# Performance work log

Measured on AMD Instinct MI355X. Metric: run time of the kernel, lower is better.

Reference implementation:

```python
import jax, jax.numpy as jnp
import numpy as np

TEMPERATURE = 0.07
EPS = 1e-12  # F.normalize eps


def _l2norm(x):
    n = jnp.linalg.norm(x, axis=-1, keepdims=True)
    return x / jnp.maximum(n, EPS)


def setup_inputs() -> dict:
    key = jax.random.key(0)
    k1, k2 = jax.random.split(key)
    B, T, H = 16, 512, 1024
    h_source = jax.random.normal(k1, (B, T, H), dtype=jnp.float32)
    h_target = jax.random.normal(k2, (B, T, H), dtype=jnp.float32)
    src_mask = jnp.ones((B, T), dtype=bool)
    tgt_mask = jnp.ones((B, T), dtype=bool)
    return {"h_source": h_source, "h_target": h_target,
            "src_mask": src_mask, "tgt_mask": tgt_mask}


def reference(h_source, h_target, src_mask, tgt_mask):
    # Masks are all-True and B*T == max_samples, so boolean selection == reshape
    # and the random subsampling branch is never taken (deterministic path).
    H = h_source.shape[-1]
    h_s = h_source.reshape(-1, H).astype(jnp.float32)          # (N, H)
    h_t = jax.lax.stop_gradient(h_target.reshape(-1, H)).astype(jnp.float32)  # detached

    h_s_norm = _l2norm(h_s)                                     # (N, H)
    h_t_norm = _l2norm(h_t)                                     # (M, H)
    sim = h_s_norm @ h_t_norm.T                                 # (N, M) cosine sim

    pos_idx = jnp.argmax(sim, axis=1)                           # == topk_idx[:, 0]
    logits = sim / TEMPERATURE
    # cross-entropy with pos_idx labels (stable log-softmax)
    logp = jax.nn.log_softmax(logits, axis=1)
    l_contrastive = -jnp.mean(jnp.take_along_axis(logp, pos_idx[:, None], axis=1)[:, 0])

    # contextual consistency: adjacent source tokens' NN embeddings should align
    nn_embeds = h_t_norm[pos_idx]                               # (N, H)
    nn_sim = jnp.sum(nn_embeds[:-1] * nn_embeds[1:], axis=-1)   # (N-1,)
    l_contextual = 1.0 - jnp.mean(nn_sim)

    return (l_contrastive, l_contextual)
```

## Files before the change

### kernel.cpp

```cpp
#include <hip/hip_runtime.h>
#include <hip/hip_bf16.h>
#include <stdint.h>


#define HDIM 1024
#define NROW 8192
#define TEMP_INV (1.0f / 0.07f)

typedef __attribute__((ext_vector_type(4))) float float4v;
typedef __attribute__((ext_vector_type(2))) float float2v;
typedef __attribute__((ext_vector_type(4))) int   int4v;
typedef __attribute__((ext_vector_type(8))) int   int8v;

#define SN_OFF   ((size_t)0)
#define TN_OFF   ((size_t)8388608)
#define TR_OFF   ((size_t)16777216)
#define SUM_OFF  ((size_t)25165824)
#define PMX_OFF  (SUM_OFF + 32768)
#define ACC_OFF  (PMX_OFF + 65536)
#define CNT_OFF  (ACC_OFF + 64)

static __device__ __forceinline__ void gload_lds16(const void* gptr, void* lptr) {
    __builtin_amdgcn_global_load_lds(
        (const __attribute__((address_space(1))) void*)gptr,
        (__attribute__((address_space(3))) void*)(uintptr_t)(uint32_t)(uintptr_t)lptr,
        16, 0, 0);
}

static __device__ __forceinline__ float fp8dot4(unsigned a, unsigned b) {
    float2v al = __builtin_amdgcn_cvt_pk_f32_fp8((int)a, false);
    float2v ah = __builtin_amdgcn_cvt_pk_f32_fp8((int)a, true);
    float2v bl = __builtin_amdgcn_cvt_pk_f32_fp8((int)b, false);
    float2v bh = __builtin_amdgcn_cvt_pk_f32_fp8((int)b, true);
    return al[0]*bl[0] + al[1]*bl[1] + ah[0]*bh[0] + ah[1]*bh[1];
}

__global__ __launch_bounds__(256)
void norm_kernel(const float* __restrict__ hs, const float* __restrict__ ht,
                 char* __restrict__ Sn, char* __restrict__ Tn, char* __restrict__ Tr,
                 float* __restrict__ sumexp, unsigned long long* __restrict__ pmax,
                 float* __restrict__ acc, unsigned* __restrict__ cnt) {
    const int b = blockIdx.x;
    const int t = threadIdx.x;
    const int wave = t >> 6, lane = t & 63;
    const bool isT = (b >= 512);
    const int g = isT ? (b - 512) : b;
    const float* in = (isT ? ht : hs) + (size_t)g * 16 * HDIM;
    char* outTiled = (isT ? Tn : Sn) + (size_t)g * 16384;

    __shared__ float sq[16][256];
    __shared__ float sscale[16];

    float4v v[16];
    #pragma unroll
    for (int i = 0; i < 16; ++i) {
        v[i] = ((const float4v*)in)[i * 256 + t];
        sq[i][t] = v[i][0]*v[i][0] + v[i][1]*v[i][1] + v[i][2]*v[i][2] + v[i][3]*v[i][3];
    }
    __syncthreads();
    #pragma unroll
    for (int j = 0; j < 4; ++j) {
        const int ri = wave * 4 + j;
        float s = sq[ri][lane] + sq[ri][lane + 64] + sq[ri][lane + 128] + sq[ri][lane + 192];
        #pragma unroll
        for (int off = 1; off < 64; off <<= 1) s += __shfl_xor(s, off);
        if (lane == 0) sscale[ri] = 1.0f / fmaxf(sqrtf(s), 1e-12f);
    }
    __syncthreads();

    char* tiled = (char*)sq;
    const int koff = (t >> 5) * 2048 + ((t >> 2) & 1) * 1024
                   + ((t >> 3) & 3) * 256 + (t & 3) * 4;
    #pragma unroll
    for (int i = 0; i < 16; ++i) {
        const float sc = sscale[i];
        int d = __builtin_amdgcn_cvt_pk_fp8_f32(v[i][0]*sc, v[i][1]*sc, 0, false);
        d     = __builtin_amdgcn_cvt_pk_fp8_f32(v[i][2]*sc, v[i][3]*sc, d, true);
        *(int*)(tiled + koff + i * 16) = d;
        if (isT) ((int*)(Tr + (size_t)(g * 16 + i) * HDIM))[t] = d;
    }
    __syncthreads();
    #pragma unroll
    for (int j = 0; j < 4; ++j)
        ((uint4*)outTiled)[j * 256 + t] = ((const uint4*)tiled)[j * 256 + t];

    if (!isT && t < 16) { sumexp[b * 16 + t] = 0.f; pmax[b * 16 + t] = 0ull; }
    if (b == 0 && t == 16) { acc[0] = 0.f; acc[1] = 0.f; *cnt = 0u; }
}

__global__ __launch_bounds__(256)
__attribute__((amdgpu_waves_per_eu(3, 3)))
void flash_kernel(const char* __restrict__ Sn, const char* __restrict__ Tn,
                  float* __restrict__ sumexp, unsigned long long* __restrict__ pmax) {
    __shared__ __align__(16) char As[16384];
    __shared__ __align__(16) char Bs[16384];
    const int t = threadIdx.x;
    const int wave = t >> 6, lane = t & 63;
    const int quad = lane >> 4, l16 = lane & 15;
    const int rbase = (int)(blockIdx.x & 63) * 128;
    const int cbase = (int)(blockIdx.x >> 6) * 128;
    const int wr = wave & 1, wc = wave >> 1;
    const int wm = wr * 64, wn = wc * 64;

    int offA[4], offB[4];
    #pragma unroll
    for (int u = 0; u < 4; ++u) {
        int ua = wave * 4 + u;
        offA[u] = (rbase / 16 + (ua >> 1)) * 16384 + (ua & 1) * 1024 + lane * 16;
        offB[u] = (cbase / 16 + (ua >> 1)) * 16384 + (ua & 1) * 1024 + lane * 16;
    }

    float4v acc[4][4];
    #pragma unroll
    for (int i = 0; i < 4; ++i)
        #pragma unroll
        for (int j = 0; j < 4; ++j) acc[i][j] = (float4v){0.f, 0.f, 0.f, 0.f};
    const int usc = 0x7f7f7f7f;

    const int aBase = wr * 4 * 2048 + lane * 16;
    const int bBase = wc * 4 * 2048 + lane * 16;

    #pragma unroll 1
    for (int kb = 0; kb < 8; ++kb) {
        const int ks = kb * 2048;
        #pragma unroll
        for (int u = 0; u < 4; ++u)
            gload_lds16(Sn + offA[u] + ks, As + (wave * 4 + u) * 1024);
        #pragma unroll
        for (int u = 0; u < 4; ++u)
            gload_lds16(Tn + offB[u] + ks, Bs + (wave * 4 + u) * 1024);
        asm volatile("s_waitcnt vmcnt(0)\ns_barrier" ::: "memory");

        int8v af[4];
        #pragma unroll
        for (int i = 0; i < 4; ++i) {
            int4v lo = *(const int4v*)(As + aBase + i * 2048);
            int4v hi = *(const int4v*)(As + aBase + i * 2048 + 1024);
            af[i] = __builtin_shufflevector(lo, hi, 0, 1, 2, 3, 4, 5, 6, 7);
        }
        __builtin_amdgcn_s_setprio(1);
        #pragma unroll
        for (int j = 0; j < 4; ++j) {
            int4v lo = *(const int4v*)(Bs + bBase + j * 2048);
            int4v hi = *(const int4v*)(Bs + bBase + j * 2048 + 1024);
            int8v bf = __builtin_shufflevector(lo, hi, 0, 1, 2, 3, 4, 5, 6, 7);
            #pragma unroll
            for (int i = 0; i < 4; ++i)
                acc[i][j] = __builtin_amdgcn_mfma_scale_f32_16x16x128_f8f6f4(
                    af[i], bf, acc[i][j], 0, 0, 0, usc, 0, usc);
        }
        __builtin_amdgcn_s_setprio(0);
        __syncthreads();
    }

    float se_v[4][4]; unsigned long long pk_v[4][4];
    #pragma unroll
    for (int i = 0; i < 4; ++i) {
        #pragma unroll
        for (int r = 0; r < 4; ++r) {
            float se = 0.f; float mx = -2.f; int mi = 0x7fffffff;
            #pragma unroll
            for (int j = 0; j < 4; ++j) {
                float v = acc[i][j][r];
                se += __expf(v * TEMP_INV);
                int col = cbase + wn + j * 16 + l16;
                if (v > mx || (v == mx && col < mi)) { mx = v; mi = col; }
            }
            #pragma unroll
            for (int off = 1; off < 16; off <<= 1) {
                se += __shfl_xor(se, off);
                float om = __shfl_xor(mx, off);
                int oi = __shfl_xor(mi, off);
                if (om > mx || (om == mx && oi < mi)) { mx = om; mi = oi; }
            }
            se_v[i][r] = se;
            pk_v[i][r] = ((unsigned long long)__float_as_uint(mx + 2.0f) << 32)
                         | (unsigned long long)(0xffffffffu - (unsigned)mi);
        }
    }
    float* pbSe = (float*)Bs;
    unsigned long long* pbPk = (unsigned long long*)(Bs + 512);
    if (wave < 2 && l16 == 0) {
        #pragma unroll
        for (int i = 0; i < 4; ++i)
            #pragma unroll
            for (int r = 0; r < 4; ++r) {
                int rl = wm + i * 16 + quad * 4 + r;
                pbSe[rl] = se_v[i][r]; pbPk[rl] = pk_v[i][r];
            }
    }
    __syncthreads();
    if (wave >= 2 && l16 == 0) {
        #pragma unroll
        for (int i = 0; i < 4; ++i)
            #pragma unroll
            for (int r = 0; r < 4; ++r) {
                int rl = wm + i * 16 + quad * 4 + r;
                float se = se_v[i][r] + pbSe[rl];
                unsigned long long pk = pk_v[i][r];
                unsigned long long po = pbPk[rl];
                if (po > pk) pk = po;
                atomicAdd(&sumexp[rbase + rl], se);
                atomicMax(&pmax[rbase + rl], pk);
            }
    }
}

__global__ __launch_bounds__(256)
void tail_kernel(const float* __restrict__ sumexp,
                 const unsigned long long* __restrict__ pmax,
                 const char* __restrict__ Tr,
                 float* __restrict__ acc, unsigned* __restrict__ cnt,
                 float* __restrict__ out) {
    const int blk = blockIdx.x;
    const int t = threadIdx.x, wave = t >> 6, lane = t & 63;

    if (wave == 0) {
        int r = blk * 32 + (lane & 31);
        unsigned long long p = pmax[r];
        float mx = __uint_as_float((unsigned)(p >> 32)) - 2.0f;
        float loss = logf(sumexp[r]) - mx * TEMP_INV;
        #pragma unroll
        for (int off = 1; off < 32; off <<= 1) loss += __shfl_xor(loss, off);
        if (lane == 0) atomicAdd(acc + 0, loss);
    }

    float s = 0.f;
    #pragma unroll
    for (int it = 0; it < 8; ++it) {
        int g = blk * 32 + wave * 8 + it;
        if (g < NROW - 1) {
            unsigned long long pa = pmax[g], pb = pmax[g + 1];
            int ia = (int)(0xffffffffu - (unsigned)(pa & 0xffffffffu));
            int ib = (int)(0xffffffffu - (unsigned)(pb & 0xffffffffu));
            uint4 va = ((const uint4*)(Tr + (size_t)ia * HDIM))[lane];
            uint4 vb = ((const uint4*)(Tr + (size_t)ib * HDIM))[lane];
            s += fp8dot4(va.x, vb.x) + fp8dot4(va.y, vb.y)
               + fp8dot4(va.z, vb.z) + fp8dot4(va.w, vb.w);
        }
    }
    #pragma unroll
    for (int off = 1; off < 64; off <<= 1) s += __shfl_xor(s, off);
    __shared__ float red[4];
    if (lane == 0) red[wave] = s;
    __syncthreads();
    if (t == 0) atomicAdd(acc + 1, red[0] + red[1] + red[2] + red[3]);

    __threadfence();
    __shared__ unsigned done;
    if (t == 0) done = atomicAdd(cnt, 1u);
    __syncthreads();
    if (t == 0 && done == 255u) {
        float l0 = atomicAdd(acc + 0, 0.0f);
        float l1 = atomicAdd(acc + 1, 0.0f);
        out[0] = l0 / (float)NROW;
        out[1] = 1.0f - l1 / (float)(NROW - 1);
    }
}

extern "C" void kernel_launch(void* const* d_in, const int* in_sizes, int n_in,
                              void* d_out, int out_size, void* d_ws, size_t ws_size,
                              hipStream_t stream) {
    const float* hs = (const float*)d_in[0];
    const float* ht = (const float*)d_in[1];
    char* ws = (char*)d_ws;
    char* Sn = ws + SN_OFF;
    char* Tn = ws + TN_OFF;
    char* Tr = ws + TR_OFF;
    float* sumexp = (float*)(ws + SUM_OFF);
    unsigned long long* pmax = (unsigned long long*)(ws + PMX_OFF);
    float* acc = (float*)(ws + ACC_OFF);
    unsigned* cnt = (unsigned*)(ws + CNT_OFF);
    float* out = (float*)d_out;

    norm_kernel<<<1024, 256, 0, stream>>>(hs, ht, Sn, Tn, Tr, sumexp, pmax, acc, cnt);
    flash_kernel<<<4096, 256, 0, stream>>>(Sn, Tn, sumexp, pmax);
    tail_kernel<<<256, 256, 0, stream>>>(sumexp, pmax, Tr, acc, cnt, out);
}
```

Before: 247.8 us.

## Load MFMA fragments directly from global memory and remap blocks per XCD

The flash kernel no longer stages A/B tiles through LDS with barriers. Each wave now loads its own fp8 fragments straight from global memory into registers, relying on the pre-tiled layout. Block indices are also remapped so blocks on the same XCD share column tiles, aiming for better L2 reuse. This removes the LDS round-trip and per-iteration barriers, but each wave now issues redundant global loads that other waves in the block also fetch, and there is no software prefetch to hide latency.

```diff
diff --git a/kernel.cpp b/kernel.cpp
--- a/kernel.cpp
+++ b/kernel.cpp
@@ -92,22 +92,28 @@
 __attribute__((amdgpu_waves_per_eu(3, 3)))
 void flash_kernel(const char* __restrict__ Sn, const char* __restrict__ Tn,
                   float* __restrict__ sumexp, unsigned long long* __restrict__ pmax) {
-    __shared__ __align__(16) char As[16384];
-    __shared__ __align__(16) char Bs[16384];
+    __shared__ float pbSe[128];
+    __shared__ unsigned long long pbPk[128];
     const int t = threadIdx.x;
     const int wave = t >> 6, lane = t & 63;
     const int quad = lane >> 4, l16 = lane & 15;
-    const int rbase = (int)(blockIdx.x & 63) * 128;
-    const int cbase = (int)(blockIdx.x >> 6) * 128;
+
+    const int bid = (int)blockIdx.x;
+    const int xcd = bid & 7;
+    const int idx = bid >> 3;
+    const int oct = idx >> 6;
+    const int w   = idx & 63;
+    const int rbase = (oct * 8 + (w & 7)) * 128;
+    const int cbase = (xcd * 8 + (w >> 3)) * 128;
+
     const int wr = wave & 1, wc = wave >> 1;
     const int wm = wr * 64, wn = wc * 64;
 
-    int offA[4], offB[4];
+    int vA[4], vB[4];
     #pragma unroll
     for (int u = 0; u < 4; ++u) {
-        int ua = wave * 4 + u;
-        offA[u] = (rbase / 16 + (ua >> 1)) * 16384 + (ua & 1) * 1024 + lane * 16;
-        offB[u] = (cbase / 16 + (ua >> 1)) * 16384 + (ua & 1) * 1024 + lane * 16;
+        vA[u] = (rbase / 16 + wr * 4 + u) * 16384 + lane * 16;
+        vB[u] = (cbase / 16 + wc * 4 + u) * 16384 + lane * 16;
     }
 
     float4v acc[4][4];
@@ -117,40 +123,34 @@
         for (int j = 0; j < 4; ++j) acc[i][j] = (float4v){0.f, 0.f, 0.f, 0.f};
     const int usc = 0x7f7f7f7f;
 
-    const int aBase = wr * 4 * 2048 + lane * 16;
-    const int bBase = wc * 4 * 2048 + lane * 16;
-
     #pragma unroll 1
     for (int kb = 0; kb < 8; ++kb) {
-        const int ks = kb * 2048;
-        #pragma unroll
-        for (int u = 0; u < 4; ++u)
-            gload_lds16(Sn + offA[u] + ks, As + (wave * 4 + u) * 1024);
-        #pragma unroll
-        for (int u = 0; u < 4; ++u)
-            gload_lds16(Tn + offB[u] + ks, Bs + (wave * 4 + u) * 1024);
-        asm volatile("s_waitcnt vmcnt(0)\ns_barrier" ::: "memory");
+        int4v alo[4], ahi[4], blo[4], bhi[4];
+        #pragma unroll
+        for (int u = 0; u < 4; ++u) {
+            alo[u] = *(const int4v*)(Sn + vA[u]);
+            ahi[u] = *(const int4v*)(Sn + vA[u] + 1024);
+        }
+        #pragma unroll
+        for (int u = 0; u < 4; ++u) {
+            blo[u] = *(const int4v*)(Tn + vB[u]);
+            bhi[u] = *(const int4v*)(Tn + vB[u] + 1024);
+        }
+        #pragma unroll
+        for (int u = 0; u < 4; ++u) { vA[u] += 2048; vB[u] += 2048; }
 
         int8v af[4];
         #pragma unroll
-        for (int i = 0; i < 4; ++i) {
-            int4v lo = *(const int4v*)(As + aBase + i * 2048);
-            int4v hi = *(const int4v*)(As + aBase + i * 2048 + 1024);
-            af[i] = __builtin_shufflevector(lo, hi, 0, 1, 2, 3, 4, 5, 6, 7);
-        }
-        __builtin_amdgcn_s_setprio(1);
+        for (int i = 0; i < 4; ++i)
+            af[i] = __builtin_shufflevector(alo[i], ahi[i], 0, 1, 2, 3, 4, 5, 6, 7);
         #pragma unroll
         for (int j = 0; j < 4; ++j) {
-            int4v lo = *(const int4v*)(Bs + bBase + j * 2048);
-            int4v hi = *(const int4v*)(Bs + bBase + j * 2048 + 1024);
-            int8v bf = __builtin_shufflevector(lo, hi, 0, 1, 2, 3, 4, 5, 6, 7);
+            int8v bf = __builtin_shufflevector(blo[j], bhi[j], 0, 1, 2, 3, 4, 5, 6, 7);
             #pragma unroll
             for (int i = 0; i < 4; ++i)
                 acc[i][j] = __builtin_amdgcn_mfma_scale_f32_16x16x128_f8f6f4(
                     af[i], bf, acc[i][j], 0, 0, 0, usc, 0, usc);
         }
-        __builtin_amdgcn_s_setprio(0);
-        __syncthreads();
     }
 
     float se_v[4][4]; unsigned long long pk_v[4][4];
@@ -178,8 +178,6 @@
                          | (unsigned long long)(0xffffffffu - (unsigned)mi);
         }
     }
-    float* pbSe = (float*)Bs;
-    unsigned long long* pbPk = (unsigned long long*)(Bs + 512);
     if (wave < 2 && l16 == 0) {
         #pragma unroll
         for (int i = 0; i < 4; ++i)
```

Result: slower. 263.8 us (+6.5%).

## Use 8 waves per flash block and XCD-aware tile mapping

Applied to the files above, without the earlier changes.

Doubles the flash kernel block to 512 threads. Each wave now computes a 64x32 sub-tile instead of 64x64, and the loader is split so four waves fetch the A tile and four fetch the B tile. Block indices are remapped so that blocks landing on the same XCD share column panels and cover an 8x8 grid of tiles, which should improve L2 reuse. The cross-wave reduction uses LDS atomics before one set of global atomics per row. In exchange there is more barrier overhead and fewer accumulators per wave, which lowers MFMA work per LDS read.

```diff
diff --git a/kernel.cpp b/kernel.cpp
--- a/kernel.cpp
+++ b/kernel.cpp
@@ -88,47 +88,57 @@
     if (b == 0 && t == 16) { acc[0] = 0.f; acc[1] = 0.f; *cnt = 0u; }
 }
 
-__global__ __launch_bounds__(256)
-__attribute__((amdgpu_waves_per_eu(3, 3)))
+__global__ __launch_bounds__(512)
+__attribute__((amdgpu_waves_per_eu(4, 4)))
 void flash_kernel(const char* __restrict__ Sn, const char* __restrict__ Tn,
                   float* __restrict__ sumexp, unsigned long long* __restrict__ pmax) {
     __shared__ __align__(16) char As[16384];
     __shared__ __align__(16) char Bs[16384];
+    __shared__ float pbSe[128];
+    __shared__ unsigned long long pbPk[128];
+
     const int t = threadIdx.x;
     const int wave = t >> 6, lane = t & 63;
     const int quad = lane >> 4, l16 = lane & 15;
-    const int rbase = (int)(blockIdx.x & 63) * 128;
-    const int cbase = (int)(blockIdx.x >> 6) * 128;
+
+    const int bid = (int)blockIdx.x;
+    const int xcd = bid & 7;
+    const int idx = bid >> 3;
+    const int oct = idx >> 6;
+    const int w   = idx & 63;
+    const int rbase = (oct * 8 + (w & 7)) * 128;
+    const int cbase = (xcd * 8 + (w >> 3)) * 128;
+
     const int wr = wave & 1, wc = wave >> 1;
-    const int wm = wr * 64, wn = wc * 64;
-
-    int offA[4], offB[4];
+
+    const bool isB = (wave >= 4);
+    const char* src = isB ? Tn : Sn;
+    char* dstBase = isB ? Bs : As;
+    const int base16 = (isB ? cbase : rbase) >> 4;
+    int off[4]; char* dst[4];
     #pragma unroll
     for (int u = 0; u < 4; ++u) {
-        int ua = wave * 4 + u;
-        offA[u] = (rbase / 16 + (ua >> 1)) * 16384 + (ua & 1) * 1024 + lane * 16;
-        offB[u] = (cbase / 16 + (ua >> 1)) * 16384 + (ua & 1) * 1024 + lane * 16;
-    }
-
-    float4v acc[4][4];
+        int uu = (wave & 3) * 4 + u;
+        off[u] = (base16 + (uu >> 1)) * 16384 + (uu & 1) * 1024 + lane * 16;
+        dst[u] = dstBase + uu * 1024;
+    }
+
+    float4v acc[4][2];
     #pragma unroll
     for (int i = 0; i < 4; ++i)
         #pragma unroll
-        for (int j = 0; j < 4; ++j) acc[i][j] = (float4v){0.f, 0.f, 0.f, 0.f};
+        for (int j = 0; j < 2; ++j) acc[i][j] = (float4v){0.f, 0.f, 0.f, 0.f};
     const int usc = 0x7f7f7f7f;
 
     const int aBase = wr * 4 * 2048 + lane * 16;
-    const int bBase = wc * 4 * 2048 + lane * 16;
+    const int bBase = wc * 2 * 2048 + lane * 16;
 
     #pragma unroll 1
     for (int kb = 0; kb < 8; ++kb) {
         const int ks = kb * 2048;
         #pragma unroll
         for (int u = 0; u < 4; ++u)
-            gload_lds16(Sn + offA[u] + ks, As + (wave * 4 + u) * 1024);
-        #pragma unroll
-        for (int u = 0; u < 4; ++u)
-            gload_lds16(Tn + offB[u] + ks, Bs + (wave * 4 + u) * 1024);
+            gload_lds16(src + off[u] + ks, dst[u]);
         asm volatile("s_waitcnt vmcnt(0)\ns_barrier" ::: "memory");
 
         int8v af[4];
@@ -140,7 +150,7 @@
         }
         __builtin_amdgcn_s_setprio(1);
         #pragma unroll
-        for (int j = 0; j < 4; ++j) {
+        for (int j = 0; j < 2; ++j) {
             int4v lo = *(const int4v*)(Bs + bBase + j * 2048);
             int4v hi = *(const int4v*)(Bs + bBase + j * 2048 + 1024);
             int8v bf = __builtin_shufflevector(lo, hi, 0, 1, 2, 3, 4, 5, 6, 7);
@@ -160,17 +170,17 @@
         for (int r = 0; r < 4; ++r) {
             float se = 0.f; float mx = -2.f; int mi = 0x7fffffff;
             #pragma unroll
-            for (int j = 0; j < 4; ++j) {
+            for (int j = 0; j < 2; ++j) {
                 float v = acc[i][j][r];
                 se += __expf(v * TEMP_INV);
-                int col = cbase + wn + j * 16 + l16;
+                int col = cbase + wc * 32 + j * 16 + l16;
                 if (v > mx || (v == mx && col < mi)) { mx = v; mi = col; }
             }
             #pragma unroll
-            for (int off = 1; off < 16; off <<= 1) {
-                se += __shfl_xor(se, off);
-                float om = __shfl_xor(mx, off);
-                int oi = __shfl_xor(mi, off);
+            for (int off2 = 1; off2 < 16; off2 <<= 1) {
+                se += __shfl_xor(se, off2);
+                float om = __shfl_xor(mx, off2);
+                int oi = __shfl_xor(mi, off2);
                 if (om > mx || (om == mx && oi < mi)) { mx = om; mi = oi; }
             }
             se_v[i][r] = se;
@@ -178,30 +188,35 @@
                          | (unsigned long long)(0xffffffffu - (unsigned)mi);
         }
     }
-    float* pbSe = (float*)Bs;
-    unsigned long long* pbPk = (unsigned long long*)(Bs + 512);
-    if (wave < 2 && l16 == 0) {
+    if (wc == 0 && l16 == 0) {
         #pragma unroll
         for (int i = 0; i < 4; ++i)
             #pragma unroll
             for (int r = 0; r < 4; ++r) {
-                int rl = wm + i * 16 + quad * 4 + r;
+                int rl = wr * 64 + i * 16 + quad * 4 + r;
                 pbSe[rl] = se_v[i][r]; pbPk[rl] = pk_v[i][r];
             }
     }
     __syncthreads();
-    if (wave >= 2 && l16 == 0) {
+    if (wc != 0 && l16 == 0) {
         #pragma unroll
         for (int i = 0; i < 4; ++i)
             #pragma unroll
             for (int r = 0; r < 4; ++r) {
-                int rl = wm + i * 16 + quad * 4 + r;
-                float se = se_v[i][r] + pbSe[rl];
-                unsigned long long pk = pk_v[i][r];
-                unsigned long long po = pbPk[rl];
-                if (po > pk) pk = po;
-                atomicAdd(&sumexp[rbase + rl], se);
-                atomicMax(&pmax[rbase + rl], pk);
+                int rl = wr * 64 + i * 16 + quad * 4 + r;
+                atomicAdd(&pbSe[rl], se_v[i][r]);
+                atomicMax(&pbPk[rl], pk_v[i][r]);
+            }
+    }
+    __syncthreads();
+    if (wc == 0 && l16 == 0) {
+        #pragma unroll
+        for (int i = 0; i < 4; ++i)
+            #pragma unroll
+            for (int r = 0; r < 4; ++r) {
+                int rl = wr * 64 + i * 16 + quad * 4 + r;
+                atomicAdd(&sumexp[rbase + rl], pbSe[rl]);
+                atomicMax(&pmax[rbase + rl], pbPk[rl]);
             }
     }
 }
@@ -274,6 +289,6 @@
     float* out = (float*)d_out;
 
     norm_kernel<<<1024, 256, 0, stream>>>(hs, ht, Sn, Tn, Tr, sumexp, pmax, acc, cnt);
-    flash_kernel<<<4096, 256, 0, stream>>>(Sn, Tn, sumexp, pmax);
+    flash_kernel<<<4096, 512, 0, stream>>>(Sn, Tn, sumexp, pmax);
     tail_kernel<<<256, 256, 0, stream>>>(sumexp, pmax, Tr, acc, cnt, out);
 }
```

After: 294.2 us. 1.19x slower.

## Use two-wave blocks with 64x128 per-wave tiles and XCD-aware block swizzle

Applied to the files above, without the earlier changes.

The flash kernel drops from 4 waves to 2 waves per 128x128 tile. Each wave now computes a 64x128 sub-tile with 32 accumulators, and one wave loads A while the other loads B. Block indices are remapped so that blocks on the same XCD share column tiles, which should improve L2 reuse. The cross-wave LDS reduction is removed and each wave issues atomics directly. This doubles the register pressure per wave and halves the wave count, and it lowers the waves-per-EU hint to 2, so latency hiding may suffer.

```diff
diff --git a/kernel.cpp b/kernel.cpp
--- a/kernel.cpp
+++ b/kernel.cpp
@@ -88,8 +88,8 @@
     if (b == 0 && t == 16) { acc[0] = 0.f; acc[1] = 0.f; *cnt = 0u; }
 }
 
-__global__ __launch_bounds__(256)
-__attribute__((amdgpu_waves_per_eu(3, 3)))
+__global__ __launch_bounds__(128)
+__attribute__((amdgpu_waves_per_eu(2, 2)))
 void flash_kernel(const char* __restrict__ Sn, const char* __restrict__ Tn,
                   float* __restrict__ sumexp, unsigned long long* __restrict__ pmax) {
     __shared__ __align__(16) char As[16384];
@@ -97,38 +97,41 @@
     const int t = threadIdx.x;
     const int wave = t >> 6, lane = t & 63;
     const int quad = lane >> 4, l16 = lane & 15;
-    const int rbase = (int)(blockIdx.x & 63) * 128;
-    const int cbase = (int)(blockIdx.x >> 6) * 128;
-    const int wr = wave & 1, wc = wave >> 1;
-    const int wm = wr * 64, wn = wc * 64;
-
-    int offA[4], offB[4];
-    #pragma unroll
-    for (int u = 0; u < 4; ++u) {
-        int ua = wave * 4 + u;
-        offA[u] = (rbase / 16 + (ua >> 1)) * 16384 + (ua & 1) * 1024 + lane * 16;
-        offB[u] = (cbase / 16 + (ua >> 1)) * 16384 + (ua & 1) * 1024 + lane * 16;
-    }
-
-    float4v acc[4][4];
+
+    const int bid = (int)blockIdx.x;
+    const int xcd = bid & 7;
+    const int idx = bid >> 3;
+    const int oct = idx >> 6;
+    const int w   = idx & 63;
+    const int rbase = (oct * 8 + (w & 7)) * 128;
+    const int cbase = (xcd * 8 + (w >> 3)) * 128;
+
+    const char* src = wave ? Tn : Sn;
+    const int base16 = (wave ? cbase : rbase) >> 4;
+    const char* gp[8];
+    #pragma unroll
+    for (int g = 0; g < 8; ++g)
+        gp[g] = src + (size_t)(base16 + g) * 16384 + lane * 16;
+    char* dstBase = wave ? Bs : As;
+
+    float4v acc[4][8];
     #pragma unroll
     for (int i = 0; i < 4; ++i)
         #pragma unroll
-        for (int j = 0; j < 4; ++j) acc[i][j] = (float4v){0.f, 0.f, 0.f, 0.f};
+        for (int j = 0; j < 8; ++j) acc[i][j] = (float4v){0.f, 0.f, 0.f, 0.f};
     const int usc = 0x7f7f7f7f;
 
-    const int aBase = wr * 4 * 2048 + lane * 16;
-    const int bBase = wc * 4 * 2048 + lane * 16;
+    const int aBase = wave * 8192 + lane * 16;
+    const int bBase = lane * 16;
 
     #pragma unroll 1
     for (int kb = 0; kb < 8; ++kb) {
         const int ks = kb * 2048;
         #pragma unroll
-        for (int u = 0; u < 4; ++u)
-            gload_lds16(Sn + offA[u] + ks, As + (wave * 4 + u) * 1024);
-        #pragma unroll
-        for (int u = 0; u < 4; ++u)
-            gload_lds16(Tn + offB[u] + ks, Bs + (wave * 4 + u) * 1024);
+        for (int g = 0; g < 8; ++g) {
+            gload_lds16(gp[g] + ks,        dstBase + g * 2048);
+            gload_lds16(gp[g] + ks + 1024, dstBase + g * 2048 + 1024);
+        }
         asm volatile("s_waitcnt vmcnt(0)\ns_barrier" ::: "memory");
 
         int8v af[4];
@@ -140,7 +143,7 @@
         }
         __builtin_amdgcn_s_setprio(1);
         #pragma unroll
-        for (int j = 0; j < 4; ++j) {
+        for (int j = 0; j < 8; ++j) {
             int4v lo = *(const int4v*)(Bs + bBase + j * 2048);
             int4v hi = *(const int4v*)(Bs + bBase + j * 2048 + 1024);
             int8v bf = __builtin_shufflevector(lo, hi, 0, 1, 2, 3, 4, 5, 6, 7);
@@ -153,17 +156,16 @@
         __syncthreads();
     }
 
-    float se_v[4][4]; unsigned long long pk_v[4][4];
     #pragma unroll
     for (int i = 0; i < 4; ++i) {
         #pragma unroll
         for (int r = 0; r < 4; ++r) {
             float se = 0.f; float mx = -2.f; int mi = 0x7fffffff;
             #pragma unroll
-            for (int j = 0; j < 4; ++j) {
+            for (int j = 0; j < 8; ++j) {
                 float v = acc[i][j][r];
                 se += __expf(v * TEMP_INV);
-                int col = cbase + wn + j * 16 + l16;
+                int col = cbase + j * 16 + l16;
                 if (v > mx || (v == mx && col < mi)) { mx = v; mi = col; }
             }
             #pragma unroll
@@ -173,36 +175,15 @@
                 int oi = __shfl_xor(mi, off);
                 if (om > mx || (om == mx && oi < mi)) { mx = om; mi = oi; }
             }
-            se_v[i][r] = se;
-            pk_v[i][r] = ((unsigned long long)__float_as_uint(mx + 2.0f) << 32)
-                         | (unsigned long long)(0xffffffffu - (unsigned)mi);
-        }
-    }
-    float* pbSe = (float*)Bs;
-    unsigned long long* pbPk = (unsigned long long*)(Bs + 512);
-    if (wave < 2 && l16 == 0) {
-        #pragma unroll
-        for (int i = 0; i < 4; ++i)
-            #pragma unroll
-            for (int r = 0; r < 4; ++r) {
-                int rl = wm + i * 16 + quad * 4 + r;
-                pbSe[rl] = se_v[i][r]; pbPk[rl] = pk_v[i][r];
+            if (l16 == 0) {
+                int row = rbase + wave * 64 + i * 16 + quad * 4 + r;
+                unsigned long long pk =
+                    ((unsigned long long)__float_as_uint(mx + 2.0f) << 32)
+                    | (unsigned long long)(0xffffffffu - (unsigned)mi);
+                atomicAdd(&sumexp[row], se);
+                atomicMax(&pmax[row], pk);
             }
-    }
-    __syncthreads();
-    if (wave >= 2 && l16 == 0) {
-        #pragma unroll
-        for (int i = 0; i < 4; ++i)
-            #pragma unroll
-            for (int r = 0; r < 4; ++r) {
-                int rl = wm + i * 16 + quad * 4 + r;
-                float se = se_v[i][r] + pbSe[rl];
-                unsigned long long pk = pk_v[i][r];
-                unsigned long long po = pbPk[rl];
-                if (po > pk) pk = po;
-                atomicAdd(&sumexp[rbase + rl], se);
-                atomicMax(&pmax[rbase + rl], pk);
-            }
+        }
     }
 }
 
@@ -274,6 +255,6 @@
     float* out = (float*)d_out;
 
     norm_kernel<<<1024, 256, 0, stream>>>(hs, ht, Sn, Tn, Tr, sumexp, pmax, acc, cnt);
-    flash_kernel<<<4096, 256, 0, stream>>>(Sn, Tn, sumexp, pmax);
+    flash_kernel<<<4096, 128, 0, stream>>>(Sn, Tn, sumexp, pmax);
     tail_kernel<<<256, 256, 0, stream>>>(sumexp, pmax, Tr, acc, cnt, out);
 }
```

Result: slower. 255.2 us (+3.0%).
